# Kernel tuning notes

Hardware: AMD Instinct MI355X
Metric: run time of the kernel (lower is better)

Reference implementation:

```python
import jax, jax.numpy as jnp
import numpy as np

B, S, T, D = 64, 50, 200, 128
IN2, H = 128, 64
NEG = -1e10


def setup_inputs() -> dict:
    key = jax.random.key(0)
    k1, k2, k3, k4, k5, k6, k7, k8 = jax.random.split(key, 8)
    inp = jax.random.normal(k1, (B, S, T, D), dtype=jnp.float32)
    z = jax.random.normal(k2, (B, S, IN2), dtype=jnp.float32)
    mask = jax.random.randint(k3, (B, S, T), 0, 2, dtype=jnp.int32)
    # torch nn.Linear weights: [out, in]
    W1 = jax.random.normal(k4, (H, D), dtype=jnp.float32) / np.sqrt(D)
    W2_w = jax.random.normal(k5, (H, IN2), dtype=jnp.float32) / np.sqrt(IN2)
    W2_b = jax.random.normal(k6, (H,), dtype=jnp.float32) * 0.01
    V_w = jax.random.normal(k7, (1, H), dtype=jnp.float32) / np.sqrt(H)
    V_b = jax.random.normal(k8, (1,), dtype=jnp.float32) * 0.01
    return {"input": inp, "z": z, "mask": mask, "W1": W1,
            "W2_w": W2_w, "W2_b": W2_b, "V_w": V_w, "V_b": V_b}


def reference(input, z, mask, W1, W2_w, W2_b, V_w, V_b):
    # w1h: [B,S,T,H]
    w1h = jnp.einsum('bstd,hd->bsth', input, W1)
    # w2h: [B,S,H] (Linear with bias), broadcast over T
    w2h = jnp.einsum('bsd,hd->bsh', z, W2_w) + W2_b
    u = jnp.tanh(w1h + w2h[:, :, None, :])           # [B,S,T,H]
    att = jnp.einsum('bsth,h->bst', u, V_w[0]) + V_b[0]  # [B,S,T]
    att = jnp.where(mask == 0, NEG, att)
    att = jax.nn.softmax(att, axis=2)
    out = jnp.einsum('bst,bstd->bsd', att, input)    # [B,S,D]
    return out
```

## Files before the change

### kernel.cpp

```cpp
#include <hip/hip_runtime.h>

#define Tdim 200
#define Ddim 128
#define Hdim 64
#define NBS  3200
#define NEGV (-1e10f)

typedef __bf16 bf16x8 __attribute__((ext_vector_type(8)));
typedef float  floatx4 __attribute__((ext_vector_type(4)));

__device__ __forceinline__ unsigned short bf16rne(float f) {
    unsigned int u = __float_as_uint(f);
    u += 0x7fffu + ((u >> 16) & 1u);
    return (unsigned short)(u >> 16);
}

__device__ __forceinline__ float ftanh(float x) {
    float e = __expf(2.0f * x);
    return 1.0f - 2.0f * __builtin_amdgcn_rcpf(e + 1.0f);
}

__global__ void prep(const float* __restrict__ z, const float* __restrict__ W2w,
                     const float* __restrict__ W2b, const float* __restrict__ W1,
                     unsigned short* __restrict__ W1bf, float* __restrict__ w2h) {
    const int tid = threadIdx.x;
    if (blockIdx.x < 800) {
        const int idx = blockIdx.x * 256 + tid;
        const int bs = idx >> 6, h = idx & 63;
        const float* zp = z + bs * 128;
        const float* wp = W2w + h * 128;
        float a = W2b[h];
        #pragma unroll 8
        for (int d = 0; d < 128; ++d) a = fmaf(zp[d], wp[d], a);
        w2h[idx] = a;
    } else {
        const int idx = (blockIdx.x - 800) * 256 + tid;
        const float4* src = (const float4*)W1 + idx * 2;
        float4 v0 = src[0], v1 = src[1];
        uint4 o;
        o.x = bf16rne(v0.x) | ((unsigned int)bf16rne(v0.y) << 16);
        o.y = bf16rne(v0.z) | ((unsigned int)bf16rne(v0.w) << 16);
        o.z = bf16rne(v1.x) | ((unsigned int)bf16rne(v1.y) << 16);
        o.w = bf16rne(v1.z) | ((unsigned int)bf16rne(v1.w) << 16);
        ((uint4*)W1bf)[idx] = o;
    }
}

__global__ __launch_bounds__(256, 3) void attn_main(
    const float* __restrict__ X, const int* __restrict__ mask,
    const float* __restrict__ Vw, const float* __restrict__ Vb,
    const unsigned short* __restrict__ W1bf, const float* __restrict__ w2h_g,
    float* __restrict__ out)
{
    __shared__ __align__(16) unsigned short xs[Tdim * 128];
    __shared__ float attL[Tdim];
    __shared__ float red[8];
    __shared__ float pp[256];

    const int tid = threadIdx.x;
    const int bs  = blockIdx.x;
    const float* __restrict__ Xb = X + (size_t)bs * (Tdim * Ddim);

    #pragma unroll 5
    for (int it = 0; it < 25; ++it) {
        int j = it * 256 + tid;
        int t = j >> 5, dq = j & 31;
        float4 v = *(const float4*)(Xb + t * Ddim + dq * 4);
        unsigned int lo = bf16rne(v.x) | ((unsigned int)bf16rne(v.y) << 16);
        unsigned int hi = bf16rne(v.z) | ((unsigned int)bf16rne(v.w) << 16);
        int u16 = t * 16 + ((dq >> 1) ^ (t & 15));
        *(uint2*)((char*)xs + u16 * 16 + (dq & 1) * 8) = make_uint2(lo, hi);
    }

    const int lane = tid & 63;
    const int wv   = tid >> 6;
    const int l15  = lane & 15, quad = lane >> 4;

    bf16x8 bfrag[4][4];
    #pragma unroll
    for (int n = 0; n < 4; ++n)
        #pragma unroll
        for (int ks = 0; ks < 4; ++ks)
            bfrag[n][ks] = *(const bf16x8*)(W1bf + (n * 16 + l15) * 128 + ks * 32 + quad * 8);

    const float Vb0 = Vb[0];
    float vw[4], w2[4];
    #pragma unroll
    for (int n = 0; n < 4; ++n) {
        int h = l15 + 16 * n;
        vw[n] = Vw[h];
        w2[n] = w2h_g[bs * 64 + h];
    }

    __syncthreads();

    for (int mt = wv; mt < 13; mt += 4) {
        const int t0 = (mt == 12) ? 184 : mt * 16;
        const int trow = t0 + l15;
        floatx4 acc[4];
        #pragma unroll
        for (int n = 0; n < 4; ++n) acc[n] = (floatx4){0.f, 0.f, 0.f, 0.f};
        bf16x8 afrag[4];
        #pragma unroll
        for (int ks = 0; ks < 4; ++ks) {
            int u16 = trow * 16 + (((ks << 2) + quad) ^ (trow & 15));
            afrag[ks] = *(const bf16x8*)(xs + u16 * 8);
        }
        #pragma unroll
        for (int n = 0; n < 4; ++n)
            #pragma unroll
            for (int ks = 0; ks < 4; ++ks)
                acc[n] = __builtin_amdgcn_mfma_f32_16x16x32_bf16(afrag[ks], bfrag[n][ks], acc[n], 0, 0, 0);

        float s0 = 0.f, s1 = 0.f, s2 = 0.f, s3 = 0.f;
        #pragma unroll
        for (int n = 0; n < 4; ++n) {
            s0 = fmaf(ftanh(acc[n][0] + w2[n]), vw[n], s0);
            s1 = fmaf(ftanh(acc[n][1] + w2[n]), vw[n], s1);
            s2 = fmaf(ftanh(acc[n][2] + w2[n]), vw[n], s2);
            s3 = fmaf(ftanh(acc[n][3] + w2[n]), vw[n], s3);
        }
        #pragma unroll
        for (int m = 1; m < 16; m <<= 1) {
            s0 += __shfl_xor(s0, m);
            s1 += __shfl_xor(s1, m);
            s2 += __shfl_xor(s2, m);
            s3 += __shfl_xor(s3, m);
        }
        if (l15 == 0) {
            const int tb = t0 + quad * 4;
            attL[tb]     = s0 + Vb0;
            attL[tb + 1] = s1 + Vb0;
            attL[tb + 2] = s2 + Vb0;
            attL[tb + 3] = s3 + Vb0;
        }
    }
    __syncthreads();

    float l = -3e38f;
    if (tid < Tdim) {
        l = attL[tid];
        if (mask[bs * Tdim + tid] == 0) l = NEGV;
    }
    float m = l;
    #pragma unroll
    for (int off = 32; off > 0; off >>= 1) m = fmaxf(m, __shfl_xor(m, off));
    if (lane == 0) red[wv] = m;
    __syncthreads();
    const float M = fmaxf(fmaxf(red[0], red[1]), fmaxf(red[2], red[3]));
    float p = __expf(l - M);
    float sm = p;
    #pragma unroll
    for (int off = 32; off > 0; off >>= 1) sm += __shfl_xor(sm, off);
    if (lane == 0) red[4 + wv] = sm;
    __syncthreads();
    const float S = (red[4] + red[5]) + (red[6] + red[7]);
    if (tid < Tdim) attL[tid] = p / S;
    __syncthreads();

    const int d = tid & 127, half = tid >> 7;
    const float* xp = Xb + half * 100 * Ddim + d;
    float o = 0.f;
    #pragma unroll 4
    for (int tt = 0; tt < 100; ++tt)
        o = fmaf(attL[half * 100 + tt], xp[tt * Ddim], o);
    pp[tid] = o;
    __syncthreads();
    if (tid < 128) out[bs * Ddim + tid] = pp[tid] + pp[tid + 128];
}

extern "C" void kernel_launch(void* const* d_in, const int* in_sizes, int n_in,
                              void* d_out, int out_size, void* d_ws, size_t ws_size,
                              hipStream_t stream) {
    const float* X    = (const float*)d_in[0];
    const float* z    = (const float*)d_in[1];
    const int*   mask = (const int*)d_in[2];
    const float* W1   = (const float*)d_in[3];
    const float* W2w  = (const float*)d_in[4];
    const float* W2b  = (const float*)d_in[5];
    const float* Vw   = (const float*)d_in[6];
    const float* Vb   = (const float*)d_in[7];
    float* out = (float*)d_out;

    unsigned short* W1bf = (unsigned short*)d_ws;
    float* w2h = (float*)((char*)d_ws + 16384);

    prep<<<804, 256, 0, stream>>>(z, W2w, W2b, W1, W1bf, w2h);
    attn_main<<<NBS, 256, 0, stream>>>(X, mask, Vw, Vb, W1bf, w2h, out);
}
```

Baseline: 504.3 us.

## Load MFMA A-fragments directly from global, drop LDS staging of X

Removes the 51KB shared-memory bf16 staging of the X tile and the barrier after it. Each wave now loads its A-fragments straight from global memory and converts them to bf16 in registers. The final weighted sum over T is rewritten to use float4 loads across 8 T-groups, reduced through shared memory. With the LDS use reduced, the launch bound rises to 4 blocks per CU, trading the coalesced staging pass for strided per-lane global reads of X.

```diff
diff --git a/kernel.cpp b/kernel.cpp
--- a/kernel.cpp
+++ b/kernel.cpp
@@ -8,6 +8,7 @@
 
 typedef __bf16 bf16x8 __attribute__((ext_vector_type(8)));
 typedef float  floatx4 __attribute__((ext_vector_type(4)));
+typedef unsigned short ushort8 __attribute__((ext_vector_type(8)));
 
 __device__ __forceinline__ unsigned short bf16rne(float f) {
     unsigned int u = __float_as_uint(f);
@@ -46,31 +47,19 @@
     }
 }
 
-__global__ __launch_bounds__(256, 3) void attn_main(
+__global__ __launch_bounds__(256, 4) void attn_main(
     const float* __restrict__ X, const int* __restrict__ mask,
     const float* __restrict__ Vw, const float* __restrict__ Vb,
     const unsigned short* __restrict__ W1bf, const float* __restrict__ w2h_g,
     float* __restrict__ out)
 {
-    __shared__ __align__(16) unsigned short xs[Tdim * 128];
     __shared__ float attL[Tdim];
     __shared__ float red[8];
-    __shared__ float pp[256];
+    __shared__ float4 pf[256];
 
     const int tid = threadIdx.x;
     const int bs  = blockIdx.x;
     const float* __restrict__ Xb = X + (size_t)bs * (Tdim * Ddim);
-
-    #pragma unroll 5
-    for (int it = 0; it < 25; ++it) {
-        int j = it * 256 + tid;
-        int t = j >> 5, dq = j & 31;
-        float4 v = *(const float4*)(Xb + t * Ddim + dq * 4);
-        unsigned int lo = bf16rne(v.x) | ((unsigned int)bf16rne(v.y) << 16);
-        unsigned int hi = bf16rne(v.z) | ((unsigned int)bf16rne(v.w) << 16);
-        int u16 = t * 16 + ((dq >> 1) ^ (t & 15));
-        *(uint2*)((char*)xs + u16 * 16 + (dq & 1) * 8) = make_uint2(lo, hi);
-    }
 
     const int lane = tid & 63;
     const int wv   = tid >> 6;
@@ -92,20 +81,27 @@
         w2[n] = w2h_g[bs * 64 + h];
     }
 
-    __syncthreads();
-
     for (int mt = wv; mt < 13; mt += 4) {
         const int t0 = (mt == 12) ? 184 : mt * 16;
         const int trow = t0 + l15;
+        const float* rp = Xb + trow * Ddim + quad * 8;
+
+        bf16x8 afrag[4];
+        #pragma unroll
+        for (int ks = 0; ks < 4; ++ks) {
+            float4 a0 = *(const float4*)(rp + ks * 32);
+            float4 a1 = *(const float4*)(rp + ks * 32 + 4);
+            ushort8 u;
+            u[0] = bf16rne(a0.x); u[1] = bf16rne(a0.y);
+            u[2] = bf16rne(a0.z); u[3] = bf16rne(a0.w);
+            u[4] = bf16rne(a1.x); u[5] = bf16rne(a1.y);
+            u[6] = bf16rne(a1.z); u[7] = bf16rne(a1.w);
+            afrag[ks] = __builtin_bit_cast(bf16x8, u);
+        }
+
         floatx4 acc[4];
         #pragma unroll
         for (int n = 0; n < 4; ++n) acc[n] = (floatx4){0.f, 0.f, 0.f, 0.f};
-        bf16x8 afrag[4];
-        #pragma unroll
-        for (int ks = 0; ks < 4; ++ks) {
-            int u16 = trow * 16 + (((ks << 2) + quad) ^ (trow & 15));
-            afrag[ks] = *(const bf16x8*)(xs + u16 * 8);
-        }
         #pragma unroll
         for (int n = 0; n < 4; ++n)
             #pragma unroll
@@ -158,15 +154,30 @@
     if (tid < Tdim) attL[tid] = p / S;
     __syncthreads();
 
-    const int d = tid & 127, half = tid >> 7;
-    const float* xp = Xb + half * 100 * Ddim + d;
-    float o = 0.f;
-    #pragma unroll 4
-    for (int tt = 0; tt < 100; ++tt)
-        o = fmaf(attL[half * 100 + tt], xp[tt * Ddim], o);
-    pp[tid] = o;
-    __syncthreads();
-    if (tid < 128) out[bs * Ddim + tid] = pp[tid] + pp[tid + 128];
+    const int c4 = tid & 31, tg = tid >> 5;
+    const float4* xp = (const float4*)Xb + c4;
+    float4 o = make_float4(0.f, 0.f, 0.f, 0.f);
+    const int tbeg = tg * 25;
+    #pragma unroll 5
+    for (int tt = tbeg; tt < tbeg + 25; ++tt) {
+        const float a = attL[tt];
+        const float4 v = xp[tt * 32];
+        o.x = fmaf(a, v.x, o.x);
+        o.y = fmaf(a, v.y, o.y);
+        o.z = fmaf(a, v.z, o.z);
+        o.w = fmaf(a, v.w, o.w);
+    }
+    pf[tg * 32 + c4] = o;
+    __syncthreads();
+    if (tid < 32) {
+        float4 s = pf[tid];
+        #pragma unroll
+        for (int g = 1; g < 8; ++g) {
+            const float4 v = pf[g * 32 + tid];
+            s.x += v.x; s.y += v.y; s.z += v.z; s.w += v.w;
+        }
+        *(float4*)(out + bs * Ddim + tid * 4) = s;
+    }
 }
 
 extern "C" void kernel_launch(void* const* d_in, const int* in_sizes, int n_in,
```

Result: no change. 512.8 us (+1.7%).

## Fuse online softmax and weighted sum into MFMA loop, drop X staging in LDS

Applied to the files above, without the earlier changes.

Each wave now loads its X tile straight from global memory into registers, converts it to bf16 for the MFMA, and reuses the same fp32 registers for an online-softmax weighted accumulation of the output. This removes the 50KB bf16 X buffer in LDS and the second pass over X from global memory. W1 is staged once in padded LDS instead of being held in registers. The cost is more registers (32 output partials per lane), a cross-lane reduction of 128 values per wave at the end, and rescaling work whenever the running max changes.

```diff
diff --git a/kernel.cpp b/kernel.cpp
--- a/kernel.cpp
+++ b/kernel.cpp
@@ -8,6 +8,7 @@
 
 typedef __bf16 bf16x8 __attribute__((ext_vector_type(8)));
 typedef float  floatx4 __attribute__((ext_vector_type(4)));
+typedef unsigned short ushort8 __attribute__((ext_vector_type(8)));
 
 __device__ __forceinline__ unsigned short bf16rne(float f) {
     unsigned int u = __float_as_uint(f);
@@ -52,36 +53,27 @@
     const unsigned short* __restrict__ W1bf, const float* __restrict__ w2h_g,
     float* __restrict__ out)
 {
-    __shared__ __align__(16) unsigned short xs[Tdim * 128];
-    __shared__ float attL[Tdim];
-    __shared__ float red[8];
-    __shared__ float pp[256];
+    __shared__ __align__(16) unsigned short w1s[64 * 136];
+    __shared__ int   maskS[Tdim];
+    __shared__ float osum[4][128];
+    __shared__ float mw[4], sw[4];
 
     const int tid = threadIdx.x;
     const int bs  = blockIdx.x;
     const float* __restrict__ Xb = X + (size_t)bs * (Tdim * Ddim);
-
-    #pragma unroll 5
-    for (int it = 0; it < 25; ++it) {
-        int j = it * 256 + tid;
-        int t = j >> 5, dq = j & 31;
-        float4 v = *(const float4*)(Xb + t * Ddim + dq * 4);
-        unsigned int lo = bf16rne(v.x) | ((unsigned int)bf16rne(v.y) << 16);
-        unsigned int hi = bf16rne(v.z) | ((unsigned int)bf16rne(v.w) << 16);
-        int u16 = t * 16 + ((dq >> 1) ^ (t & 15));
-        *(uint2*)((char*)xs + u16 * 16 + (dq & 1) * 8) = make_uint2(lo, hi);
-    }
-
-    const int lane = tid & 63;
-    const int wv   = tid >> 6;
-    const int l15  = lane & 15, quad = lane >> 4;
-
-    bf16x8 bfrag[4][4];
-    #pragma unroll
-    for (int n = 0; n < 4; ++n)
-        #pragma unroll
-        for (int ks = 0; ks < 4; ++ks)
-            bfrag[n][ks] = *(const bf16x8*)(W1bf + (n * 16 + l15) * 128 + ks * 32 + quad * 8);
+    const int lane = tid & 63, wv = tid >> 6;
+    const int l15 = lane & 15, quad = lane >> 4;
+
+    {
+        const uint4* src = (const uint4*)W1bf;
+        #pragma unroll
+        for (int r = 0; r < 4; ++r) {
+            int u = r * 256 + tid;
+            int h = u >> 4, i = u & 15;
+            *(uint4*)((char*)w1s + h * 272 + i * 16) = src[u];
+        }
+    }
+    if (tid < Tdim) maskS[tid] = mask[bs * Tdim + tid];
 
     const float Vb0 = Vb[0];
     float vw[4], w2[4];
@@ -91,26 +83,44 @@
         vw[n] = Vw[h];
         w2[n] = w2h_g[bs * 64 + h];
     }
-
     __syncthreads();
+
+    float m_run = -3e38f, s_lane = 0.f;
+    float opart[4][8];
+    #pragma unroll
+    for (int ks = 0; ks < 4; ++ks)
+        #pragma unroll
+        for (int j = 0; j < 8; ++j) opart[ks][j] = 0.f;
 
     for (int mt = wv; mt < 13; mt += 4) {
         const int t0 = (mt == 12) ? 184 : mt * 16;
         const int trow = t0 + l15;
+        const float* rp = Xb + trow * Ddim + quad * 8;
+
+        float4 a0[4], a1[4];
+        #pragma unroll
+        for (int ks = 0; ks < 4; ++ks) {
+            a0[ks] = *(const float4*)(rp + ks * 32);
+            a1[ks] = *(const float4*)(rp + ks * 32 + 4);
+        }
+
         floatx4 acc[4];
         #pragma unroll
         for (int n = 0; n < 4; ++n) acc[n] = (floatx4){0.f, 0.f, 0.f, 0.f};
-        bf16x8 afrag[4];
         #pragma unroll
         for (int ks = 0; ks < 4; ++ks) {
-            int u16 = trow * 16 + (((ks << 2) + quad) ^ (trow & 15));
-            afrag[ks] = *(const bf16x8*)(xs + u16 * 8);
-        }
-        #pragma unroll
-        for (int n = 0; n < 4; ++n)
+            ushort8 u;
+            u[0] = bf16rne(a0[ks].x); u[1] = bf16rne(a0[ks].y);
+            u[2] = bf16rne(a0[ks].z); u[3] = bf16rne(a0[ks].w);
+            u[4] = bf16rne(a1[ks].x); u[5] = bf16rne(a1[ks].y);
+            u[6] = bf16rne(a1[ks].z); u[7] = bf16rne(a1[ks].w);
+            const bf16x8 af = __builtin_bit_cast(bf16x8, u);
             #pragma unroll
-            for (int ks = 0; ks < 4; ++ks)
-                acc[n] = __builtin_amdgcn_mfma_f32_16x16x32_bf16(afrag[ks], bfrag[n][ks], acc[n], 0, 0, 0);
+            for (int n = 0; n < 4; ++n) {
+                const bf16x8 bf = *(const bf16x8*)((char*)w1s + (n * 16 + l15) * 272 + ks * 64 + quad * 16);
+                acc[n] = __builtin_amdgcn_mfma_f32_16x16x32_bf16(af, bf, acc[n], 0, 0, 0);
+            }
+        }
 
         float s0 = 0.f, s1 = 0.f, s2 = 0.f, s3 = 0.f;
         #pragma unroll
@@ -127,46 +137,64 @@
             s2 += __shfl_xor(s2, m);
             s3 += __shfl_xor(s3, m);
         }
-        if (l15 == 0) {
-            const int tb = t0 + quad * 4;
-            attL[tb]     = s0 + Vb0;
-            attL[tb + 1] = s1 + Vb0;
-            attL[tb + 2] = s2 + Vb0;
-            attL[tb + 3] = s3 + Vb0;
-        }
-    }
+        const int src = (l15 >> 2) << 4;
+        const float b0 = __shfl(s0, src), b1 = __shfl(s1, src);
+        const float b2 = __shfl(s2, src), b3 = __shfl(s3, src);
+        float lg = (l15 & 2) ? ((l15 & 1) ? b3 : b2) : ((l15 & 1) ? b1 : b0);
+        lg += Vb0;
+        if ((mt == 12) && (l15 < 8)) lg = -3e38f;
+        else if (maskS[trow] == 0)   lg = NEGV;
+
+        float tm = lg;
+        #pragma unroll
+        for (int m = 1; m < 16; m <<= 1) tm = fmaxf(tm, __shfl_xor(tm, m));
+        const float m_new = fmaxf(m_run, tm);
+        if (m_new > m_run) {
+            const float alpha = __expf(m_run - m_new);
+            s_lane *= alpha;
+            #pragma unroll
+            for (int ks = 0; ks < 4; ++ks)
+                #pragma unroll
+                for (int j = 0; j < 8; ++j) opart[ks][j] *= alpha;
+            m_run = m_new;
+        }
+        const float p = __expf(lg - m_run);
+        s_lane += p;
+        #pragma unroll
+        for (int ks = 0; ks < 4; ++ks) {
+            opart[ks][0] = fmaf(p, a0[ks].x, opart[ks][0]);
+            opart[ks][1] = fmaf(p, a0[ks].y, opart[ks][1]);
+            opart[ks][2] = fmaf(p, a0[ks].z, opart[ks][2]);
+            opart[ks][3] = fmaf(p, a0[ks].w, opart[ks][3]);
+            opart[ks][4] = fmaf(p, a1[ks].x, opart[ks][4]);
+            opart[ks][5] = fmaf(p, a1[ks].y, opart[ks][5]);
+            opart[ks][6] = fmaf(p, a1[ks].z, opart[ks][6]);
+            opart[ks][7] = fmaf(p, a1[ks].w, opart[ks][7]);
+        }
+    }
+
+    float S_w = s_lane;
+    #pragma unroll
+    for (int m = 1; m < 16; m <<= 1) S_w += __shfl_xor(S_w, m);
+    if (lane == 0) { mw[wv] = m_run; sw[wv] = S_w; }
     __syncthreads();
-
-    float l = -3e38f;
-    if (tid < Tdim) {
-        l = attL[tid];
-        if (mask[bs * Tdim + tid] == 0) l = NEGV;
-    }
-    float m = l;
-    #pragma unroll
-    for (int off = 32; off > 0; off >>= 1) m = fmaxf(m, __shfl_xor(m, off));
-    if (lane == 0) red[wv] = m;
+    const float M = fmaxf(fmaxf(mw[0], mw[1]), fmaxf(mw[2], mw[3]));
+    const float Stot = sw[0] * __expf(mw[0] - M) + sw[1] * __expf(mw[1] - M)
+                     + sw[2] * __expf(mw[2] - M) + sw[3] * __expf(mw[3] - M);
+    const float beta = __expf(m_run - M) * __builtin_amdgcn_rcpf(Stot);
+
+    #pragma unroll
+    for (int ks = 0; ks < 4; ++ks)
+        #pragma unroll
+        for (int j = 0; j < 8; ++j) {
+            float v = opart[ks][j] * beta;
+            #pragma unroll
+            for (int m = 1; m < 16; m <<= 1) v += __shfl_xor(v, m);
+            if (l15 == 0) osum[wv][ks * 32 + quad * 8 + j] = v;
+        }
     __syncthreads();
-    const float M = fmaxf(fmaxf(red[0], red[1]), fmaxf(red[2], red[3]));
-    float p = __expf(l - M);
-    float sm = p;
-    #pragma unroll
-    for (int off = 32; off > 0; off >>= 1) sm += __shfl_xor(sm, off);
-    if (lane == 0) red[4 + wv] = sm;
-    __syncthreads();
-    const float S = (red[4] + red[5]) + (red[6] + red[7]);
-    if (tid < Tdim) attL[tid] = p / S;
-    __syncthreads();
-
-    const int d = tid & 127, half = tid >> 7;
-    const float* xp = Xb + half * 100 * Ddim + d;
-    float o = 0.f;
-    #pragma unroll 4
-    for (int tt = 0; tt < 100; ++tt)
-        o = fmaf(attL[half * 100 + tt], xp[tt * Ddim], o);
-    pp[tid] = o;
-    __syncthreads();
-    if (tid < 128) out[bs * Ddim + tid] = pp[tid] + pp[tid + 128];
+    if (tid < 128)
+        out[bs * Ddim + tid] = (osum[0][tid] + osum[1][tid]) + (osum[2][tid] + osum[3][tid]);
 }
 
 extern "C" void kernel_launch(void* const* d_in, const int* in_sizes, int n_in,
```

Measured after the change: 508.3 us. About the same (+0.8%).
